# Kernel tuning notes

Measured on AMD Instinct MI355X. Metric: run time of the kernel, lower is better.

## Reference

```python
import jax, jax.numpy as jnp
import numpy as np

NUM_TOKENS = 32
PAD_TOKEN = 1
DEL_COST = 1.0
INF = 1e9
EPS = 1e-7


def setup_inputs() -> dict:
    key = jax.random.key(0)
    k1, k2 = jax.random.split(key)
    y_true = jax.random.randint(k1, (32, 512), 0, NUM_TOKENS)
    y_pred = jax.random.uniform(k2, (32, 1024, NUM_TOKENS), dtype=jnp.float32)
    return {"y_true": y_true, "y_pred": y_pred}


def _left_shift(seq, pad_token):
    # remove internal pad tokens, shift real tokens left (stable)
    L = seq.shape[1]
    ixs = jnp.arange(L)
    keys = jnp.where(seq != pad_token, ixs[None, :], L + ixs[None, :])
    order = jnp.sort(keys, axis=1) % L
    return jnp.take_along_axis(seq, order, axis=1)


def _alignment(subs, ins, seq_lens):
    # subs: [b, m, n] substitution costs; ins: [b, n] insertion costs
    b, m, n = subs.shape
    dt = subs.dtype

    # wavefrontify subs -> [m+n-1, m, b]: out[k, i, :] = subs[:, i, k-i] (0 if oob)
    ks = jnp.arange(m + n - 1)[:, None]
    ii = jnp.arange(m)[None, :]
    jj = ks - ii
    subs_t = jnp.transpose(subs, (1, 2, 0))  # [m, n, b]
    subs_wf = jnp.where((jj >= 0) & (jj < n)[..., None] if False else ((jj >= 0) & (jj < n))[..., None],
                        subs_t[ii, jnp.clip(jj, 0, n - 1)], jnp.zeros((), dt))

    # wavefrontify ins -> [m+n, m+1, b]: out[k, i, :] = ins[:, k-i] (0 if oob)
    ks2 = jnp.arange(m + n)[:, None]
    ii2 = jnp.arange(m + 1)[None, :]
    jj2 = ks2 - ii2
    ins_t = jnp.transpose(ins, (1, 0))  # [n, b]
    ins_wf = jnp.where(((jj2 >= 0) & (jj2 < n))[..., None],
                       ins_t[jnp.clip(jj2, 0, n - 1)], jnp.zeros((), dt))

    i_range = jnp.arange(m + 1)
    batch_idx = jnp.arange(b)
    k_end = seq_lens + n  # antidiagonal where each sequence's answer lives

    # k=0 wavefront: D[0][0]=0 ; k=1 wavefront: D[0][1]=ins[0], D[1][0]=del
    v_p2 = jnp.concatenate([jnp.zeros((1, b), dt), jnp.full((m - 1, b), INF, dt)], 0)
    v_p1 = jnp.concatenate([ins_wf[0][:1], jnp.full((1, b), DEL_COST, dt),
                            jnp.full((m - 1, b), INF, dt)], 0)
    v_opt = jnp.full((b,), INF, dt)

    def step(carry, xs):
        v_p2, v_p1, v_opt = carry
        k, sub_k, ins_k = xs
        o_m = v_p2 + sub_k            # match:  D[i][j] + subs -> row i+1
        o_i = v_p1 + ins_k            # insert: D[i][j-1] + ins[j-1]
        v_p2n = v_p1[:-1]
        o_d = v_p2n + DEL_COST        # delete: D[i-1][j] + del
        rest = jnp.minimum(jnp.minimum(o_m, o_i[1:]), o_d)
        v_p1n = jnp.concatenate([o_i[:1], rest], 0)
        mask = ((k - i_range) >= 0) & ((k - i_range) <= n)
        v_p1n = jnp.where(mask[:, None], v_p1n, jnp.full((), INF, dt))
        v_opt = jnp.where(k_end == k, v_p1n[seq_lens, batch_idx], v_opt)
        return (v_p2n, v_p1n, v_opt), None

    ks_seq = jnp.arange(2, m + n + 1)
    (_, _, v_opt), _ = jax.lax.scan(step, (v_p2, v_p1, v_opt),
                                    (ks_seq, subs_wf, ins_wf[1:]))
    return v_opt


def reference(y_true, y_pred):
    y_true_ls = _left_shift(y_true, PAD_TOKEN)
    seq_lens = jnp.sum((y_true_ls != PAD_TOKEN).astype(jnp.int32), axis=-1)
    y_oh = jax.nn.one_hot(y_true_ls, NUM_TOKENS, dtype=y_pred.dtype)
    y_p = y_pred / jnp.sum(y_pred, axis=-1, keepdims=True)
    logp = jnp.log(jnp.clip(y_p, EPS, 1.0 - EPS))  # [b, n, t]
    subs = -jnp.einsum('bmt,bnt->bmn', y_oh, logp)  # sparse xent cost matrix
    ins = -jnp.log(jnp.clip(y_p[..., PAD_TOKEN], EPS, 1.0 - EPS))  # [b, n]
    loss = _alignment(subs, ins, seq_lens)
    return loss.sum()  # reduction='sum'
```

## Files before the change

### kernel.cpp

```cpp
#include <hip/hip_runtime.h>

#define NTOK 32
#define PADT 1
#define MLEN 512
#define NLEN 1024
#define EPS_F 1e-7f

#define RCH 128
#define NC  4
#define NWAVE 4
#define NPHASE (NC + NWAVE - 1)

#define OFF_P0   0
#define OFF_BND  1024
#define OFF_BNDZ (OFF_BND + 6*256)
#define OFF_TOK  (OFF_BNDZ + 256)
#define OFF_WT   (OFF_TOK + 736)
#define OFF_NL   (OFF_WT + 16)
#define LDS_FLOATS (OFF_NL + NTOK*NLEN)

__device__ __forceinline__ float min3f(float a, float b, float c) {
  return fminf(fminf(a, b), c);
}
__device__ __forceinline__ float dpp_shr1(float old_v, float src) {
  return __int_as_float(__builtin_amdgcn_update_dpp(
      __float_as_int(old_v), __float_as_int(src), 0x138, 0xF, 0xF, false));
}

template <bool MASKED>
__device__ __forceinline__ void do_iter(
    int s0, int lane, int wv,
    const int* __restrict__ tokl, const float* __restrict__ nlJ,
    const float* __restrict__ bndR, float* __restrict__ bndW,
    int (&TKc)[8], float4 (&SBc)[8], int (&TKn)[8], float4 (&SBn)[8],
    float4 ri,
    float& vp0, float& vp1, float& vp2, float& vp3,
    float& dgL, float& m3p,
    float& wq0, float& wq1, float& wq2, float& wq3,
    float& ans, int qh)
{
#pragma unroll
  for (int k = 0; k < 8; ++k) TKn[k] = tokl[s0 + 16 + k];
#pragma unroll
  for (int k = 0; k < 8; ++k)
    SBn[k] = *(const float4*)(nlJ + ((size_t)((unsigned)TKc[k]) << 10));
  float4 ja = *(const float4*)(bndR + s0);
  float4 jb = *(const float4*)(bndR + s0 + 4);
  float inj[8] = {ja.x, ja.y, ja.z, ja.w, jb.x, jb.y, jb.z, jb.w};
  const int q0 = s0 - lane;
#pragma unroll
  for (int k = 0; k < 8; ++k) {
    const int q = q0 + k;
    float Lnow = dpp_shr1(inj[k], m3p);
    float m0 = min3f(dgL + SBc[k].x, vp0 + 1.0f, Lnow + ri.x);
    float m1 = min3f(vp0 + SBc[k].y, vp1 + 1.0f, m0 + ri.y);
    float m2 = min3f(vp1 + SBc[k].z, vp2 + 1.0f, m1 + ri.z);
    float m3 = min3f(vp2 + SBc[k].w, vp3 + 1.0f, m2 + ri.w);
    if (MASKED) {
      bool act = ((unsigned)q) < 128u;
      bool lt  = (q < 128);
      dgL = lt ? Lnow : dgL;
      vp0 = act ? m0 : vp0;  vp1 = act ? m1 : vp1;
      vp2 = act ? m2 : vp2;  vp3 = act ? m3 : vp3;
      m3p = act ? m3 : m3p;
      if (act && q == qh) ans = m3;
    } else {
      dgL = Lnow; vp0 = m0; vp1 = m1; vp2 = m2; vp3 = m3; m3p = m3;
      if (q == qh) ans = m3;
    }
    switch ((k + 1) & 3) {
      case 0: wq0 = m3; break; case 1: wq1 = m3; break;
      case 2: wq2 = m3; break; case 3: wq3 = m3; break;
    }
    if (k == 2 || k == 6) {
      int q63 = s0 + k - 63;
      if (wv < 3 && lane == 63 && q63 >= 3 && q63 < 128)
        *(float4*)(bndW + (q63 - 3)) = make_float4(wq0, wq1, wq2, wq3);
    }
  }
}

__global__ __launch_bounds__(256, 1) void align_loss_kernel(
    const int* __restrict__ y_true, const float* __restrict__ y_pred,
    float* __restrict__ partial)
{
  extern __shared__ float smem[];
  float* P0    = smem + OFF_P0;
  float* bnd   = smem + OFF_BND;
  float* bndZ  = smem + OFF_BNDZ;
  int*   tokbuf= (int*)(smem + OFF_TOK);
  int*   tokg  = tokbuf + 64;
  float* wtmp  = smem + OFF_WT;
  int*   wti   = (int*)wtmp;
  float* nl    = smem + OFF_NL;

  const int b = blockIdx.x;
  const int t = threadIdx.x;
  const int lane = t & 63;
  const int wv = t >> 6;

  for (int idx = t; idx < 736; idx += 256) tokbuf[idx] = 0;
  __syncthreads();

  int total = 0;
  for (int h = 0; h < 2; ++h) {
    int yt = y_true[b * MLEN + h * 256 + t];
    bool f = (yt != PADT);
    unsigned long long m = __ballot(f);
    int wp = __popcll(m & ((1ull << lane) - 1ull));
    if (lane == 0) wti[8 + wv] = __popcll(m);
    __syncthreads();
    int offs = total, ht = 0;
#pragma unroll
    for (int w2 = 0; w2 < NWAVE; ++w2) { int cnt = wti[8 + w2]; if (w2 < wv) offs += cnt; ht += cnt; }
    if (f) tokg[offs + wp] = yt;
    total += ht;
    __syncthreads();
  }
  const int L = total;

  for (int r = t; r < NLEN; r += 256) {
    const float4* rp = (const float4*)(y_pred + ((size_t)b * NLEN + r) * NTOK);
    float4 q[8]; float s = 0.f;
#pragma unroll
    for (int u = 0; u < 8; ++u) { q[u] = rp[u]; s += q[u].x + q[u].y + q[u].z + q[u].w; }
    float inv = 1.0f / s;
#pragma unroll
    for (int u = 0; u < 8; ++u) {
      float pv[4] = {q[u].x, q[u].y, q[u].z, q[u].w};
#pragma unroll
      for (int c2 = 0; c2 < 4; ++c2) {
        float p = pv[c2] * inv;
        p = fminf(fmaxf(p, EPS_F), 1.0f - EPS_F);
        nl[(u * 4 + c2) * NLEN + r] = -__logf(p);
      }
    }
  }
  __syncthreads();

  {
    float4 iv = *(const float4*)(nl + PADT * NLEN + 4 * t);
    float p1 = iv.x, p2 = iv.x + iv.y, p3 = p2 + iv.z, s4 = p3 + iv.w;
    float x = s4;
#pragma unroll
    for (int d = 1; d < 64; d <<= 1) {
      float y = __shfl_up(x, d);
      if (lane >= d) x += y;
    }
    if (lane == 63) wtmp[wv] = x;
    __syncthreads();
    float pre = x - s4;
#pragma unroll
    for (int w2 = 0; w2 < NWAVE; ++w2) if (w2 < wv) pre += wtmp[w2];
    *(float4*)(P0 + 4 * t) = make_float4(pre + p1, pre + p2, pre + p3, pre + s4);
  }
  __syncthreads();

  const int J = 256 * wv + 4 * lane;
  const float* nlJ = nl + J;
  float4 ri = *(const float4*)(nl + PADT * NLEN + J);
  float4 vpi = *(const float4*)(P0 + J);
  float vp0 = vpi.x, vp1 = vpi.y, vp2 = vpi.z, vp3 = vpi.w;
  float m3p = vp3;
  float dgL = 0.0f;
  if (J > 0) dgL = P0[J - 1];
  float wq0 = 0, wq1 = 0, wq2 = 0, wq3 = 0, ans = 0.0f;

  for (int p = 0; p < NPHASE; ++p) {
    __syncthreads();
    const int c = p - wv;
    if (c < 0 || c >= NC) continue;
    const int* tokl = tokg + c * RCH - lane;
    const float* bndR = (wv == 0) ? bndZ : (bnd + ((wv - 1) * 2 + (c & 1)) * 256);
    float* bndW = bnd + (wv * 2 + (c & 1)) * 256;
    const int qh = L - 1 - c * RCH;
    if (wv == 0) {
      float base = (float)(c * RCH + 1);
      bndZ[lane]       = base + (float)lane;
      bndZ[lane + 64]  = base + (float)(lane + 64);
      bndZ[lane + 128] = base + (float)(lane + 128);
      bndZ[lane + 192] = base + (float)(lane + 192);
    }
    int tk0[8], TKa[8], TKb[8]; float4 SBa[8], SBb[8];
#pragma unroll
    for (int k = 0; k < 8; ++k) tk0[k] = tokl[k];
#pragma unroll
    for (int k = 0; k < 8; ++k) SBa[k] = *(const float4*)(nlJ + ((size_t)((unsigned)tk0[k]) << 10));
#pragma unroll
    for (int k = 0; k < 8; ++k) TKa[k] = tokl[8 + k];

    int s0 = 0;
    for (int pr = 0; pr < 4; ++pr) {
      do_iter<true>(s0, lane, wv, tokl, nlJ, bndR, bndW, TKa, SBa, TKb, SBb, ri,
                    vp0, vp1, vp2, vp3, dgL, m3p, wq0, wq1, wq2, wq3, ans, qh); s0 += 8;
      do_iter<true>(s0, lane, wv, tokl, nlJ, bndR, bndW, TKb, SBb, TKa, SBa, ri,
                    vp0, vp1, vp2, vp3, dgL, m3p, wq0, wq1, wq2, wq3, ans, qh); s0 += 8;
    }
    for (int pr = 0; pr < 4; ++pr) {
      do_iter<false>(s0, lane, wv, tokl, nlJ, bndR, bndW, TKa, SBa, TKb, SBb, ri,
                     vp0, vp1, vp2, vp3, dgL, m3p, wq0, wq1, wq2, wq3, ans, qh); s0 += 8;
      do_iter<false>(s0, lane, wv, tokl, nlJ, bndR, bndW, TKb, SBb, TKa, SBa, ri,
                     vp0, vp1, vp2, vp3, dgL, m3p, wq0, wq1, wq2, wq3, ans, qh); s0 += 8;
    }
    for (int pr = 0; pr < 4; ++pr) {
      do_iter<true>(s0, lane, wv, tokl, nlJ, bndR, bndW, TKa, SBa, TKb, SBb, ri,
                    vp0, vp1, vp2, vp3, dgL, m3p, wq0, wq1, wq2, wq3, ans, qh); s0 += 8;
      do_iter<true>(s0, lane, wv, tokl, nlJ, bndR, bndW, TKb, SBb, TKa, SBa, ri,
                    vp0, vp1, vp2, vp3, dgL, m3p, wq0, wq1, wq2, wq3, ans, qh); s0 += 8;
    }
  }

  if (t == 255) partial[b] = ans;
  if (L == 0 && t == 0) partial[b] = P0[NLEN - 1];
}

__global__ void reduce_kernel(const float* __restrict__ partial, float* __restrict__ out) {
  if (threadIdx.x == 0) {
    float s = 0.f;
    for (int b2 = 0; b2 < 32; ++b2) s += partial[b2];
    out[0] = s;
  }
}

extern "C" void kernel_launch(void* const* d_in, const int* in_sizes, int n_in,
                              void* d_out, int out_size, void* d_ws, size_t ws_size,
                              hipStream_t stream) {
  const int*   y_true = (const int*)d_in[0];
  const float* y_pred = (const float*)d_in[1];
  float* out = (float*)d_out;
  float* partial = (float*)d_ws;

  const size_t lds_bytes = (size_t)LDS_FLOATS * sizeof(float);
  hipFuncSetAttribute((const void*)align_loss_kernel,
                      hipFuncAttributeMaxDynamicSharedMemorySize, (int)lds_bytes);

  hipLaunchKernelGGL(align_loss_kernel, dim3(32), dim3(256), lds_bytes, stream,
                     y_true, y_pred, partial);
  hipLaunchKernelGGL(reduce_kernel, dim3(1), dim3(64), 0, stream, partial, out);
}
```

Measured before the change: 97.52 us.

## Pack tokens as bytes, prefetch boundary values, compute wave-0 boundary in registers

Tokens are now stored as bytes in LDS and read as dwords, with byte-funnel extraction done in registers. This cuts the per-iteration token LDS loads from eight to two. Boundary inputs for the next 8-step chunk are prefetched one iteration ahead, and wave 0 computes its boundary values arithmetically instead of reading them from an LDS buffer. Wave 3 now writes its boundary output to a scratch area, which removes a branch. The cost is more register pressure and some extra shift and extract ALU work in the serial DP loop.

```diff
diff --git a/kernel.cpp b/kernel.cpp
--- a/kernel.cpp
+++ b/kernel.cpp
@@ -11,13 +11,13 @@
 #define NWAVE 4
 #define NPHASE (NC + NWAVE - 1)
 
-#define OFF_P0   0
-#define OFF_BND  1024
-#define OFF_BNDZ (OFF_BND + 6*256)
-#define OFF_TOK  (OFF_BNDZ + 256)
-#define OFF_WT   (OFF_TOK + 736)
-#define OFF_NL   (OFF_WT + 16)
-#define LDS_FLOATS (OFF_NL + NTOK*NLEN)
+#define OFF_P0    0
+#define OFF_BND   1024
+#define OFF_TOKB  (OFF_BND + 6*256)
+#define OFF_WT    (OFF_TOKB + 224)
+#define OFF_NL    (OFF_WT + 16)
+#define OFF_SCR   (OFF_NL + NTOK*NLEN)
+#define LDS_FLOATS (OFF_SCR + 256)
 
 __device__ __forceinline__ float min3f(float a, float b, float c) {
   return fminf(fminf(a, b), c);
@@ -26,32 +26,52 @@
   return __int_as_float(__builtin_amdgcn_update_dpp(
       __float_as_int(old_v), __float_as_int(src), 0x138, 0xF, 0xF, false));
 }
+__device__ __forceinline__ unsigned fbyte(unsigned lo, unsigned hi, int a0) {
+  return (unsigned)(((((unsigned long long)hi) << 32) | lo) >> (8 * a0));
+}
 
 template <bool MASKED>
 __device__ __forceinline__ void do_iter(
-    int s0, int lane, int wv,
-    const int* __restrict__ tokl, const float* __restrict__ nlJ,
+    int s0, int lane, bool wzero,
+    const int* __restrict__ tokd, int& dn,
+    const float* __restrict__ nlJ,
     const float* __restrict__ bndR, float* __restrict__ bndW,
-    int (&TKc)[8], float4 (&SBc)[8], int (&TKn)[8], float4 (&SBn)[8],
-    float4 ri,
+    int a0, int& W0, int& W1, int& W2,
+    unsigned XKc0, unsigned XKc1, unsigned& XKn0, unsigned& XKn1,
+    float4 (&SBc)[8], float (&INJc)[8],
+    float4 (&SBn)[8], float (&INJn)[8],
+    float4 ri, float cbase,
     float& vp0, float& vp1, float& vp2, float& vp3,
     float& dgL, float& m3p,
     float& wq0, float& wq1, float& wq2, float& wq3,
     float& ans, int qh)
 {
-#pragma unroll
-  for (int k = 0; k < 8; ++k) TKn[k] = tokl[s0 + 16 + k];
-#pragma unroll
-  for (int k = 0; k < 8; ++k)
-    SBn[k] = *(const float4*)(nlJ + ((size_t)((unsigned)TKc[k]) << 10));
-  float4 ja = *(const float4*)(bndR + s0);
-  float4 jb = *(const float4*)(bndR + s0 + 4);
-  float inj[8] = {ja.x, ja.y, ja.z, ja.w, jb.x, jb.y, jb.z, jb.w};
+  int Wa = tokd[dn];
+  int Wb = tokd[dn + 1];
+#pragma unroll
+  for (int k = 0; k < 4; ++k)
+    SBn[k] = *(const float4*)(nlJ + ((size_t)((XKc0 >> (8 * k)) & 0xFFu) << 10));
+#pragma unroll
+  for (int k = 0; k < 4; ++k)
+    SBn[4 + k] = *(const float4*)(nlJ + ((size_t)((XKc1 >> (8 * k)) & 0xFFu) << 10));
+  if (wzero) {
+    float f = cbase + (float)(s0 + 8);
+#pragma unroll
+    for (int k = 0; k < 8; ++k) INJn[k] = f + (float)k;
+  } else {
+    float4 ja = *(const float4*)(bndR + s0 + 8);
+    float4 jb = *(const float4*)(bndR + s0 + 12);
+    INJn[0] = ja.x; INJn[1] = ja.y; INJn[2] = ja.z; INJn[3] = ja.w;
+    INJn[4] = jb.x; INJn[5] = jb.y; INJn[6] = jb.z; INJn[7] = jb.w;
+  }
+  XKn0 = fbyte((unsigned)W0, (unsigned)W1, a0);
+  XKn1 = fbyte((unsigned)W1, (unsigned)W2, a0);
+
   const int q0 = s0 - lane;
 #pragma unroll
   for (int k = 0; k < 8; ++k) {
     const int q = q0 + k;
-    float Lnow = dpp_shr1(inj[k], m3p);
+    float Lnow = dpp_shr1(INJc[k], m3p);
     float m0 = min3f(dgL + SBc[k].x, vp0 + 1.0f, Lnow + ri.x);
     float m1 = min3f(vp0 + SBc[k].y, vp1 + 1.0f, m0 + ri.y);
     float m2 = min3f(vp1 + SBc[k].z, vp2 + 1.0f, m1 + ri.z);
@@ -74,10 +94,11 @@
     }
     if (k == 2 || k == 6) {
       int q63 = s0 + k - 63;
-      if (wv < 3 && lane == 63 && q63 >= 3 && q63 < 128)
+      if (lane == 63 && q63 >= 3 && q63 < 128)
         *(float4*)(bndW + (q63 - 3)) = make_float4(wq0, wq1, wq2, wq3);
     }
   }
+  W0 = W2; W1 = Wa; W2 = Wb; dn += 2;
 }
 
 __global__ __launch_bounds__(256, 1) void align_loss_kernel(
@@ -87,19 +108,20 @@
   extern __shared__ float smem[];
   float* P0    = smem + OFF_P0;
   float* bnd   = smem + OFF_BND;
-  float* bndZ  = smem + OFF_BNDZ;
-  int*   tokbuf= (int*)(smem + OFF_TOK);
-  int*   tokg  = tokbuf + 64;
+  unsigned char* tokb = (unsigned char*)(smem + OFF_TOKB);
+  const int* tokd = (const int*)(smem + OFF_TOKB);
   float* wtmp  = smem + OFF_WT;
   int*   wti   = (int*)wtmp;
   float* nl    = smem + OFF_NL;
+  float* scr   = smem + OFF_SCR;
 
   const int b = blockIdx.x;
   const int t = threadIdx.x;
   const int lane = t & 63;
   const int wv = t >> 6;
-
-  for (int idx = t; idx < 736; idx += 256) tokbuf[idx] = 0;
+  const bool wzero = (wv == 0);
+
+  if (t < 224) ((int*)tokb)[t] = 0;
   __syncthreads();
 
   int total = 0;
@@ -113,7 +135,7 @@
     int offs = total, ht = 0;
 #pragma unroll
     for (int w2 = 0; w2 < NWAVE; ++w2) { int cnt = wti[8 + w2]; if (w2 < wv) offs += cnt; ht += cnt; }
-    if (f) tokg[offs + wp] = yt;
+    if (f) tokb[64 + offs + wp] = (unsigned char)yt;
     total += ht;
     __syncthreads();
   }
@@ -170,44 +192,52 @@
     __syncthreads();
     const int c = p - wv;
     if (c < 0 || c >= NC) continue;
-    const int* tokl = tokg + c * RCH - lane;
-    const float* bndR = (wv == 0) ? bndZ : (bnd + ((wv - 1) * 2 + (c & 1)) * 256);
-    float* bndW = bnd + (wv * 2 + (c & 1)) * 256;
+    const float* bndR = wzero ? P0 : (bnd + ((wv - 1) * 2 + (c & 1)) * 256);
+    float* bndW = (wv < 3) ? (bnd + (wv * 2 + (c & 1)) * 256) : scr;
     const int qh = L - 1 - c * RCH;
-    if (wv == 0) {
-      float base = (float)(c * RCH + 1);
-      bndZ[lane]       = base + (float)lane;
-      bndZ[lane + 64]  = base + (float)(lane + 64);
-      bndZ[lane + 128] = base + (float)(lane + 128);
-      bndZ[lane + 192] = base + (float)(lane + 192);
-    }
-    int tk0[8], TKa[8], TKb[8]; float4 SBa[8], SBb[8];
-#pragma unroll
-    for (int k = 0; k < 8; ++k) tk0[k] = tokl[k];
-#pragma unroll
-    for (int k = 0; k < 8; ++k) SBa[k] = *(const float4*)(nlJ + ((size_t)((unsigned)tk0[k]) << 10));
-#pragma unroll
-    for (int k = 0; k < 8; ++k) TKa[k] = tokl[8 + k];
+    const float cbase = (float)(c * RCH + 1);
+
+    const int B0buf = 64 + c * RCH - lane;
+    const int a0 = B0buf & 3;
+    int dn = B0buf >> 2;
+    int D0 = tokd[dn], D1 = tokd[dn+1], D2 = tokd[dn+2], D3 = tokd[dn+3],
+        D4 = tokd[dn+4], D5 = tokd[dn+5], D6 = tokd[dn+6];
+    unsigned XA0 = fbyte((unsigned)D0, (unsigned)D1, a0);
+    unsigned XA1 = fbyte((unsigned)D1, (unsigned)D2, a0);
+    unsigned XKc0 = fbyte((unsigned)D2, (unsigned)D3, a0);
+    unsigned XKc1 = fbyte((unsigned)D3, (unsigned)D4, a0);
+    float4 SBc[8], SBn[8]; float INJc[8], INJn[8];
+    unsigned XKn0, XKn1;
+#pragma unroll
+    for (int k = 0; k < 4; ++k)
+      SBc[k] = *(const float4*)(nlJ + ((size_t)((XA0 >> (8 * k)) & 0xFFu) << 10));
+#pragma unroll
+    for (int k = 0; k < 4; ++k)
+      SBc[4 + k] = *(const float4*)(nlJ + ((size_t)((XA1 >> (8 * k)) & 0xFFu) << 10));
+    if (wzero) {
+#pragma unroll
+      for (int k = 0; k < 8; ++k) INJc[k] = cbase + (float)k;
+    } else {
+      float4 ja = *(const float4*)(bndR);
+      float4 jb = *(const float4*)(bndR + 4);
+      INJc[0] = ja.x; INJc[1] = ja.y; INJc[2] = ja.z; INJc[3] = ja.w;
+      INJc[4] = jb.x; INJc[5] = jb.y; INJc[6] = jb.z; INJc[7] = jb.w;
+    }
+    int W0 = D4, W1 = D5, W2 = D6; dn += 7;
 
     int s0 = 0;
-    for (int pr = 0; pr < 4; ++pr) {
-      do_iter<true>(s0, lane, wv, tokl, nlJ, bndR, bndW, TKa, SBa, TKb, SBb, ri,
-                    vp0, vp1, vp2, vp3, dgL, m3p, wq0, wq1, wq2, wq3, ans, qh); s0 += 8;
-      do_iter<true>(s0, lane, wv, tokl, nlJ, bndR, bndW, TKb, SBb, TKa, SBa, ri,
-                    vp0, vp1, vp2, vp3, dgL, m3p, wq0, wq1, wq2, wq3, ans, qh); s0 += 8;
-    }
-    for (int pr = 0; pr < 4; ++pr) {
-      do_iter<false>(s0, lane, wv, tokl, nlJ, bndR, bndW, TKa, SBa, TKb, SBb, ri,
-                     vp0, vp1, vp2, vp3, dgL, m3p, wq0, wq1, wq2, wq3, ans, qh); s0 += 8;
-      do_iter<false>(s0, lane, wv, tokl, nlJ, bndR, bndW, TKb, SBb, TKa, SBa, ri,
-                     vp0, vp1, vp2, vp3, dgL, m3p, wq0, wq1, wq2, wq3, ans, qh); s0 += 8;
-    }
-    for (int pr = 0; pr < 4; ++pr) {
-      do_iter<true>(s0, lane, wv, tokl, nlJ, bndR, bndW, TKa, SBa, TKb, SBb, ri,
-                    vp0, vp1, vp2, vp3, dgL, m3p, wq0, wq1, wq2, wq3, ans, qh); s0 += 8;
-      do_iter<true>(s0, lane, wv, tokl, nlJ, bndR, bndW, TKb, SBb, TKa, SBa, ri,
-                    vp0, vp1, vp2, vp3, dgL, m3p, wq0, wq1, wq2, wq3, ans, qh); s0 += 8;
-    }
+#define ITER_AB(M) \
+    do_iter<M>(s0, lane, wzero, tokd, dn, nlJ, bndR, bndW, a0, W0, W1, W2, \
+               XKc0, XKc1, XKn0, XKn1, SBc, INJc, SBn, INJn, ri, cbase, \
+               vp0, vp1, vp2, vp3, dgL, m3p, wq0, wq1, wq2, wq3, ans, qh); s0 += 8; \
+    do_iter<M>(s0, lane, wzero, tokd, dn, nlJ, bndR, bndW, a0, W0, W1, W2, \
+               XKn0, XKn1, XKc0, XKc1, SBn, INJn, SBc, INJc, ri, cbase, \
+               vp0, vp1, vp2, vp3, dgL, m3p, wq0, wq1, wq2, wq3, ans, qh); s0 += 8;
+
+    for (int pr = 0; pr < 4; ++pr) { ITER_AB(true) }
+    for (int pr = 0; pr < 4; ++pr) { ITER_AB(false) }
+    for (int pr = 0; pr < 4; ++pr) { ITER_AB(true) }
+#undef ITER_AB
   }
 
   if (t == 255) partial[b] = ans;
```

Result: slower. 110.4 us (+13.2%).
